# Optimization experiments

Measured on AMD Instinct MI355X. Metric: run time of the kernel, lower is better.

The kernel has to match this reference:

```python
import jax, jax.numpy as jnp
import numpy as np
from jax import lax

C_LIGHT = 3e8
SPATIAL, CROP = 64, 128
BIN_LEN, WALL, SAMP_COEFF, CYCLES = 0.01, 2.0, 2.0, 5
B, D = 2, 1


def _waveconvparam(bin_resolution, virtual_wavelength, cycles):
    samples = int(round(cycles * virtual_wavelength / (C_LIGHT * bin_resolution)))
    num_cycles = samples * (C_LIGHT * bin_resolution) / virtual_wavelength
    sigma = 0.3
    g = np.arange(samples, dtype=np.float64)
    env = np.exp(-(((g - samples / 2.0) / (samples / 2.0)) ** 2) / (2 * sigma ** 2))
    cos_k = np.cos(2 * np.pi * num_cycles * g / samples) * env
    sin_k = np.sin(2 * np.pi * num_cycles * g / samples) * env
    return cos_k, sin_k


def _define_psf(N, M, slope):
    # LCT psf: locus of min |(4 slope)^2 (x^2+y^2) - z|, normalized and circularly shifted
    x = np.arange(2 * N, dtype=np.float64) / (2 * N - 1) * 2 - 1
    z = np.arange(2 * M, dtype=np.float64) / (2 * M - 1) * 2
    gy, gx, gz = np.meshgrid(x, x, z)  # (2N,2N,2M)
    blur = np.abs((4 * slope) ** 2 * (gx ** 2 + gy ** 2) - gz)
    d = (np.abs(blur - blur.min(axis=2, keepdims=True)) < 1e-8).astype(np.float64)
    e = d / np.sqrt(d.sum())
    f = np.roll(np.roll(e, N, axis=0), N, axis=1)
    return np.transpose(f, (2, 0, 1))  # (2M,2N,2N)


def _resampling_operator(M):
    row = M * M
    x = np.arange(1, row + 1, dtype=np.float64)
    mtx = np.zeros((row, M), dtype=np.float64)
    mtx[np.arange(row), np.ceil(np.sqrt(x)).astype(np.int64) - 1] = 1.0
    mtx = mtx / np.sqrt(x)[:, None]
    mtxi = mtx.T.copy()
    for _ in range(int(np.log2(M))):
        mtx = 0.5 * (mtx[0::2] + mtx[1::2])
        mtxi = 0.5 * (mtxi[:, 0::2] + mtxi[:, 1::2])
    return mtx.astype(np.float32), mtxi.astype(np.float32)


def setup_inputs() -> dict:
    key = jax.random.key(0)
    kf, kw, kb = jax.random.split(key, 3)
    bin_res = BIN_LEN / C_LIGHT
    trange = CROP * C_LIGHT * bin_res
    slope = (WALL / 2.0) / trange
    vlam = SAMP_COEFF * 2.0 * (WALL / (SPATIAL - 1))
    cos_k, sin_k = _waveconvparam(bin_res, vlam, CYCLES)
    wave = np.stack([cos_k, sin_k], 0)[:, ::-1][:, None, :].astype(np.float32)  # (2,1,k)
    psf = _define_psf(SPATIAL, CROP, slope)
    invpsf = np.conj(np.fft.fftn(psf))
    mtx, mtxi = _resampling_operator(CROP)
    return {
        "feature": jax.random.normal(kf, (B, D, CROP, SPATIAL, SPATIAL), jnp.float32),
        "conv_w": jax.random.normal(kw, ()) * 0.1 + 1.0,
        "conv_b": jax.random.normal(kb, ()) * 0.1,
        "wave": jnp.asarray(wave),
        "invpsf_real": jnp.asarray(np.real(invpsf).astype(np.float32))[None],
        "invpsf_imag": jnp.asarray(np.imag(invpsf).astype(np.float32))[None],
        "mtx": jnp.asarray(mtx),
        "mtxi": jnp.asarray(mtxi),
    }


def _attention(k1, k2, w, b):
    # SE-style cross attention; Conv3d(1,1,1) on unbatched (C=1,T,H,W) is w*x+b
    T = k2.shape[1]
    pe = jnp.sin(jnp.arange(T, dtype=k2.dtype))  # PE3D with 1 channel -> sin along T
    k2p = k2 + pe[None, :, None, None]
    scal = jnp.mean(w * k1 + b)  # conv + adaptive_avg_pool3d(1), channel dim = 1
    q = (w * k2p + b).reshape(1, 1, -1)
    attn = jax.nn.sigmoid(jax.nn.softmax(scal * q, axis=2)).reshape(k2p.shape)
    return attn * k2p


def _fre_atten2(kernel, w, b):
    _, T, H, W = kernel.shape
    ct, ch, cw = T // 2, H // 2, W // 2
    st, sh, sw = (T - ct) // 2, (H - ch) // 2, (W - cw) // 2
    sl = (slice(None), slice(ct - st, ct + st), slice(ch - sh, ch + sh), slice(cw - sw, cw + sw))
    high = kernel[sl]
    low = jnp.roll(kernel, (ct, ch, cw), axis=(1, 2, 3))[sl]
    l2l = _attention(low, low, w, b)
    l2h = _attention(l2l, high, w, b)
    temp = kernel.at[sl].set(l2h)
    temp = jnp.roll(temp, (ct, ch, cw), axis=(1, 2, 3)).at[sl].set(l2l)
    return jnp.roll(temp, (ct, ch, cw), axis=(1, 2, 3))


def _forward(feature, conv_w, conv_b, wave, invpsf_real, invpsf_imag, mtx, mtxi):
    b, d, T, H, W = feature.shape
    BD = b * d
    k = wave.shape[2]
    # virtual wave conv along time: (BDHW,1,T) x (2,1,k)
    data = feature.reshape(BD, T, H, W).transpose(0, 2, 3, 1).reshape(-1, 1, T)
    conv = lax.conv_general_dilated(data, wave, (1,), [(k // 2, k // 2)],
                                    dimension_numbers=("NCH", "OIH", "NCH"))
    if k % 2 == 0:
        conv = conv[:, :, 1:]
    data2 = conv.reshape(BD, H, W, 2, T).transpose(3, 0, 4, 1, 2).reshape(2 * BD, T, H, W)
    # temporal resampling then zero-pad to 2T,2H,2W
    tmp = jnp.einsum("tm,bmx->btx", mtx, data2.reshape(2 * BD, T, H * W)).reshape(2 * BD, T, H, W)
    datapad = jnp.zeros((2 * BD, 2 * T, 2 * H, 2 * W), feature.dtype).at[:, :T, :H, :W].set(tmp)
    datafre = jnp.fft.fftn(datapad)  # torch.fft.fftn transforms ALL dims incl. batch
    w1 = _fre_atten2(invpsf_real, conv_w, conv_b)
    w2 = _fre_atten2(invpsf_imag, conv_w, conv_b)
    re_real = datafre.real * w1 - datafre.imag * w2
    re_imag = datafre.real * w2 + datafre.imag * w1
    re = jnp.fft.ifftn(lax.complex(re_real, re_imag))
    vol = re[:, :T, :H, :W]
    cr, ci = vol[:BD].real, vol[:BD].imag
    sr, si = vol[BD:].real, vol[BD:].imag
    sum_real = cr ** 2 - ci ** 2 + sr ** 2 - si ** 2
    sum_imag = 2 * cr * ci + 2 * sr * si
    mag = jax.nn.relu((jnp.sqrt(sum_real ** 2 + sum_imag ** 2) + sum_real) * 0.5)
    sq = jnp.sqrt(mag)
    out = jnp.einsum("tm,bmx->btx", mtxi, sq.reshape(BD, T, H * W))
    return out.reshape(b, d, T, H, W)


def reference(feature, conv_w, conv_b, wave, invpsf_real, invpsf_imag, mtx, mtxi):
    return _forward(feature, conv_w, conv_b, wave, invpsf_real, invpsf_imag, mtx, mtxi)
```

## Files before the change

kernel.cpp:

```cpp
#include <hip/hip_runtime.h>

#define BLKE 524288
#define VOLE 4194304
#define TCROP 2097152
#define PI2 6.283185307179586476925286766559

__device__ __forceinline__ float2 cmulf(float2 a, float2 b){
  return make_float2(a.x*b.x - a.y*b.y, a.x*b.y + a.y*b.x);
}
__device__ __forceinline__ float waveSum(float v){
  #pragma unroll
  for (int o=32;o;o>>=1) v += __shfl_xor(v,o);
  return v;
}
__device__ __forceinline__ float waveMaxf(float v){
  #pragma unroll
  for (int o=32;o;o>>=1) v = fmaxf(v,__shfl_xor(v,o));
  return v;
}
__device__ __forceinline__ float waveMinf(float v){
  #pragma unroll
  for (int o=32;o;o>>=1) v = fminf(v,__shfl_xor(v,o));
  return v;
}

__device__ __forceinline__ void bcastReduce5(const float* __restrict__ pA, int kap,
    float& sum, float& mnl, float& mxl, float& mnh, float& mxh, float* sm ){
  int tid = threadIdx.x;
  const float* q = pA + kap*1280 + tid*5;
  float s = q[0], a = q[1], b = q[2], c = q[3], d = q[4];
  s = waveSum(s); a = waveMinf(a); b = waveMaxf(b); c = waveMinf(c); d = waveMaxf(d);
  if ((tid&63)==0){ int w = tid>>6; sm[w]=s; sm[4+w]=a; sm[8+w]=b; sm[12+w]=c; sm[16+w]=d; }
  __syncthreads();
  sum = sm[0]+sm[1]+sm[2]+sm[3];
  mnl = fminf(fminf(sm[4],sm[5]),fminf(sm[6],sm[7]));
  mxl = fmaxf(fmaxf(sm[8],sm[9]),fmaxf(sm[10],sm[11]));
  mnh = fminf(fminf(sm[12],sm[13]),fminf(sm[14],sm[15]));
  mxh = fmaxf(fmaxf(sm[16],sm[17]),fmaxf(sm[18],sm[19]));
}

__device__ __forceinline__ float bcastSum256(const float* __restrict__ p, float* sm ){
  int tid = threadIdx.x;
  float s = waveSum(p[tid]);
  if ((tid&63)==0) sm[tid>>6] = s;
  __syncthreads();
  return sm[0]+sm[1]+sm[2]+sm[3];
}

__global__ void __launch_bounds__(256) kD1(const float* __restrict__ mtx,
                                           const float* __restrict__ wave,
                                           float* __restrict__ M,
                                           const float* __restrict__ Kr,
                                           const float* __restrict__ Ki,
                                           float* __restrict__ Lw, float* __restrict__ Hw,
                                           float* __restrict__ pA){
  __shared__ float spe[128];
  __shared__ float sm[20];
  int bid = blockIdx.x;
  int tid = threadIdx.x;
  if (bid < 512){
    int kap = bid >> 8, bx = bid & 255;
    const float* K = kap ? Ki : Kr;
    if (tid < 128) spe[tid] = sinf((float)tid);
    __syncthreads();
    float sum=0.f, mnl=3.4e38f, mxl=-3.4e38f, mnh=3.4e38f, mxh=-3.4e38f;
    int base = bx*256 + tid;
    #pragma unroll
    for (int it = 0; it < 8; it++){
      int e = base + it*65536;
      int tau = e >> 12, rem = e & 4095, eta = rem >> 6, om = rem & 63;
      float pe = spe[tau];
      float lo = K[(size_t)((tau+192)&255)*16384 + ((eta+96)&127)*128 + ((om+96)&127)];
      float hi = K[(size_t)(tau+64)*16384 + (eta+32)*128 + (om+32)];
      sum += lo;
      float lp = lo+pe, hp = hi+pe;
      Lw[kap*BLKE + e] = lp;
      Hw[kap*BLKE + e] = hp;
      mnl=fminf(mnl,lp); mxl=fmaxf(mxl,lp);
      mnh=fminf(mnh,hp); mxh=fmaxf(mxh,hp);
    }
    sum = waveSum(sum); mnl=waveMinf(mnl); mxl=waveMaxf(mxl); mnh=waveMinf(mnh); mxh=waveMaxf(mxh);
    if ((tid&63)==0){ int w=tid>>6; sm[w]=sum; sm[4+w]=mnl; sm[8+w]=mxl; sm[12+w]=mnh; sm[16+w]=mxh; }
    __syncthreads();
    if (tid==0){
      float* o = pA + kap*1280 + bx*5;
      o[0] = sm[0]+sm[1]+sm[2]+sm[3];
      o[1] = fminf(fminf(sm[4],sm[5]),fminf(sm[6],sm[7]));
      o[2] = fmaxf(fmaxf(sm[8],sm[9]),fmaxf(sm[10],sm[11]));
      o[3] = fminf(fminf(sm[12],sm[13]),fminf(sm[14],sm[15]));
      o[4] = fmaxf(fmaxf(sm[16],sm[17]),fmaxf(sm[18],sm[19]));
    }
  } else {
    int idx = (bid-512)*256 + tid;
    int o = idx >> 14, r = idx & 16383;
    int t = r >> 7, s = r & 127;
    float acc = 0.f;
    int mlo = s-31; if (mlo < 0) mlo = 0;
    int mhi = s+31; if (mhi > 127) mhi = 127;
    for (int m = mlo; m <= mhi; m++) acc += mtx[t*128+m]*wave[o*63 + (s-m+31)];
    M[idx] = acc;
  }
}

__global__ void __launch_bounds__(256) kD2(const float* __restrict__ feat,
                                           const float* __restrict__ M,
                                           float* __restrict__ tmp,
                                           const float* __restrict__ pA,
                                           const float* __restrict__ Lw,
                                           float* __restrict__ pB,
                                           const float* cw, const float* cb){
  __shared__ __align__(16) char smem[16640];
  __shared__ float sm[20], smo[4];
  int bid = blockIdx.x;
  int tid = threadIdx.x;
  if (bid < 512){
    int kap = bid >> 8, bx = bid & 255;
    float sum,mnl,mxl,mnh,mxh;
    bcastReduce5(pA,kap,sum,mnl,mxl,mnh,mxh,sm);
    float w = cw[0], b = cb[0];
    float s1 = w*(sum*(1.0f/BLKE)) + b;
    float a1 = s1*w, c1 = s1*b;
    float mx = (a1>=0.f) ? a1*mxl+c1 : a1*mnl+c1;
    float acc = 0.f;
    int base = kap*BLKE + bx*256 + tid;
    #pragma unroll
    for (int it = 0; it < 8; it++){
      float lp = Lw[base + it*65536];
      acc += expf(a1*lp + c1 - mx);
    }
    acc = waveSum(acc);
    if ((tid&63)==0) smo[tid>>6] = acc;
    __syncthreads();
    if (tid==0) pB[kap*256 + bx] = smo[0]+smo[1]+smo[2]+smo[3];
  } else {
    int e = bid - 512;
    int b = e >> 8, tt = (e >> 6) & 3, xt = e & 63;
    float (*LF)[64] = (float(*)[64])smem;
    float (*LM)[32][33] = (float(*)[32][33])(smem + 8192);
    int xx = tid & 63, tq = tid >> 6;
    float acc0[8] = {}, acc1[8] = {};
    const float* fb = feat + (size_t)b*BLKE;
    for (int sb = 0; sb < 4; sb++){
      #pragma unroll
      for (int j = 0; j < 8; j++){
        int idx = tid + j*256; int s = idx >> 6, x = idx & 63;
        LF[s][x] = fb[(size_t)(sb*32+s)*4096 + xt*64 + x];
      }
      #pragma unroll
      for (int j = 0; j < 8; j++){
        int idx = tid + j*256; int o = idx >> 10, r = idx & 1023;
        int trow = r >> 5, s = r & 31;
        LM[o][trow][s] = M[o*16384 + (tt*32+trow)*128 + sb*32+s];
      }
      __syncthreads();
      for (int s = 0; s < 32; s++){
        float f = LF[s][xx];
        #pragma unroll
        for (int i = 0; i < 8; i++){
          acc0[i] += LM[0][tq*8+i][s]*f;
          acc1[i] += LM[1][tq*8+i][s]*f;
        }
      }
      __syncthreads();
    }
    #pragma unroll
    for (int i = 0; i < 8; i++){
      int t = tt*32 + tq*8 + i;
      tmp[(size_t)(0*2+b)*BLKE + (size_t)t*4096 + xt*64+xx] = acc0[i];
      tmp[(size_t)(1*2+b)*BLKE + (size_t)t*4096 + xt*64+xx] = acc1[i];
    }
  }
}

__global__ void __launch_bounds__(256) kD3(const float* __restrict__ tmp,
                                           float2* __restrict__ Z2,
                                           const float* __restrict__ pA,
                                           const float* __restrict__ pB,
                                           const float* __restrict__ Lw,
                                           float* __restrict__ pC,
                                           const float* cw, const float* cb){
  __shared__ __align__(16) char smem[8832];
  __shared__ float sm[20], smB[4], smo[4];
  int bid = blockIdx.x;
  int tid = threadIdx.x;
  if (bid < 512){
    int kap = bid >> 8, bx = bid & 255;
    float sum,mnl,mxl,mnh,mxh;
    bcastReduce5(pA,kap,sum,mnl,mxl,mnh,mxh,sm);
    float d1 = bcastSum256(pB + kap*256, smB);
    float w = cw[0], b = cb[0];
    float s1 = w*(sum*(1.0f/BLKE)) + b;
    float a1 = s1*w, c1 = s1*b;
    float mx = (a1>=0.f) ? a1*mxl+c1 : a1*mnl+c1;
    float invd = 1.0f/d1;
    float acc = 0.f;
    int base = kap*BLKE + bx*256 + tid;
    #pragma unroll
    for (int it = 0; it < 8; it++){
      float lp = Lw[base + it*65536];
      float p = expf(a1*lp + c1 - mx)*invd;
      acc += lp/(1.f + expf(-p));
    }
    acc = waveSum(acc);
    if ((tid&63)==0) smo[tid>>6] = acc;
    __syncthreads();
    if (tid==0) pC[kap*256 + bx] = smo[0]+smo[1]+smo[2]+smo[3];
  } else {
    int e = bid - 512;
    int b = e >> 11, bx = e & 2047;
    float2 (*bA)[130] = (float2(*)[130])smem;
    float2 (*bB)[130] = (float2(*)[130])(smem + 4160);
    float2* tw = (float2*)(smem + 8320);
    if (tid < 64){
      double ang = -PI2 * (double)tid / 128.0;
      tw[tid] = make_float2((float)cos(ang), (float)sin(ang));
    }
    int l = tid >> 6, lane = tid & 63;
    int line = bx*4 + l;
    int t = line >> 6, h = line & 63;
    const float* pc = tmp + (size_t)b*BLKE + (size_t)t*4096 + h*64;
    const float* ps = tmp + (size_t)(2+b)*BLKE + (size_t)t*4096 + h*64;
    bA[l][lane] = make_float2(pc[lane], ps[lane]);
    bA[l][lane+64] = make_float2(0.f, 0.f);
    __syncthreads();
    float2 (*src)[130] = bA, (*dst)[130] = bB;
    int m = 1;
    #pragma unroll
    for (int st = 0; st < 7; st++){
      int i = lane;
      int jm = i & ~(m-1);
      float2 a = src[l][i], b2 = src[l][i+64];
      float2 s = make_float2(a.x+b2.x, a.y+b2.y);
      float2 d = make_float2(a.x-b2.x, a.y-b2.y);
      dst[l][i+jm]   = s;
      dst[l][i+jm+m] = cmulf(d, tw[jm]);
      __syncthreads();
      float2 (*tp)[130] = src; src = dst; dst = tp;
      m <<= 1;
    }
    float2* outp = Z2 + (size_t)b*TCROP + (size_t)t*16384 + (size_t)h*128;
    outp[lane]    = src[l][lane];
    outp[lane+64] = src[l][lane+64];
  }
}

__global__ void __launch_bounds__(256) kD4(float2* __restrict__ Z2,
                                           const float* __restrict__ pA,
                                           const float* __restrict__ pC,
                                           const float* __restrict__ Hw,
                                           float* __restrict__ pD,
                                           const float* cw, const float* cb){
  __shared__ __align__(16) char smem[33792];
  __shared__ float sm[20], smC[4], smo[4];
  int bid = blockIdx.x;
  int tid = threadIdx.x;
  if (bid < 512){
    int kap = bid >> 8, bx = bid & 255;
    float sum,mnl,mxl,mnh,mxh;
    bcastReduce5(pA,kap,sum,mnl,mxl,mnh,mxh,sm);
    float sl2 = bcastSum256(pC + kap*256, smC);
    float w = cw[0], b = cb[0];
    float s2 = w*(sl2*(1.0f/BLKE)) + b;
    float a2 = s2*w, c2 = s2*b;
    float mx = (a2>=0.f) ? a2*mxh+c2 : a2*mnh+c2;
    float acc = 0.f;
    int base = kap*BLKE + bx*256 + tid;
    #pragma unroll
    for (int it = 0; it < 8; it++){
      float hp = Hw[base + it*65536];
      acc += expf(a2*hp + c2 - mx);
    }
    acc = waveSum(acc);
    if ((tid&63)==0) smo[tid>>6] = acc;
    __syncthreads();
    if (tid==0) pD[kap*256 + bx] = smo[0]+smo[1]+smo[2]+smo[3];
  } else {
    int e = bid - 512;
    int b = e >> 10, bx = e & 1023;
    float2 (*bA)[130] = (float2(*)[130])smem;
    float2 (*bB)[130] = (float2(*)[130])(smem + 16640);
    float2* tw = (float2*)(smem + 33280);
    if (tid < 64){
      double ang = -PI2 * (double)tid / 128.0;
      tw[tid] = make_float2((float)cos(ang), (float)sin(ang));
    }
    float2* Z = Z2 + (size_t)b*TCROP;
    int t = bx >> 3; int w0 = (bx & 7) << 4;
    size_t base = (size_t)t*16384 + w0;
    #pragma unroll
    for (int q = 0; q < 4; q++){
      int idx = q*256 + tid; int wl = idx & 15, hh = idx >> 4;
      bA[wl][hh] = Z[base + (size_t)hh*128 + wl];
      bA[wl][hh+64] = make_float2(0.f, 0.f);
    }
    __syncthreads();
    float2 (*src)[130] = bA, (*dst)[130] = bB;
    int m = 1;
    #pragma unroll
    for (int st = 0; st < 7; st++){
      #pragma unroll
      for (int q = 0; q < 4; q++){
        int g = q*256 + tid; int li = g >> 6; int i = g & 63;
        int jm = i & ~(m-1);
        float2 a = src[li][i], b2 = src[li][i+64];
        float2 s = make_float2(a.x+b2.x, a.y+b2.y);
        float2 d = make_float2(a.x-b2.x, a.y-b2.y);
        dst[li][i+jm]   = s;
        dst[li][i+jm+m] = cmulf(d, tw[jm]);
      }
      __syncthreads();
      float2 (*tp)[130] = src; src = dst; dst = tp;
      m <<= 1;
    }
    #pragma unroll
    for (int q = 0; q < 8; q++){
      int idx = q*256 + tid; int wl = idx & 15, hh = idx >> 4;
      Z[base + (size_t)hh*128 + wl] = src[wl][hh];
    }
  }
}

__device__ __forceinline__ float attnv(float v, float a, float c, float mx, float invd){
  float p = expf(a*v + c - mx)*invd;
  return v / (1.f + expf(-p));
}
__device__ __forceinline__ float2 wcAt(int t, int h, int w,
                                       const float* __restrict__ Kr, const float* __restrict__ Ki,
                                       const float* spe, const float* P){
  size_t off = (size_t)t*16384 + (size_t)h*128 + w;
  float kr = Kr[off], ki = Ki[off];
  bool center = (t>=64 && t<192) && (h>=32 && h<96) && (w>=32 && w<96);
  int tc = (t+64)&255, hc = (h+32)&127, wc = (w+32)&127;
  bool corner = (tc<128) && (hc<64) && (wc<64);
  float2 o;
  if (center){
    float pe = spe[t-64];
    o.x = attnv(kr+pe, P[4],  P[5],  P[6],  P[7]);
    o.y = attnv(ki+pe, P[12], P[13], P[14], P[15]);
  } else if (corner){
    float pe = spe[tc];
    o.x = attnv(kr+pe, P[0], P[1],  P[2],  P[3]);
    o.y = attnv(ki+pe, P[8], P[9],  P[10], P[11]);
  } else {
    o.x = kr; o.y = ki;
  }
  return o;
}

__global__ void __launch_bounds__(256) kWcF(const float* __restrict__ Kr,
                                            const float* __restrict__ Ki,
                                            const float* __restrict__ pA,
                                            const float* __restrict__ pB,
                                            const float* __restrict__ pC,
                                            const float* __restrict__ pD,
                                            const float* cw, const float* cb,
                                            float2* __restrict__ Wc){
  __shared__ float spe[128];
  __shared__ float P[16];
  __shared__ float sm[20], smB[4], smC[4], smD[4];
  int tid = threadIdx.x;
  if (tid < 128) spe[tid] = sinf((float)tid);
  for (int kap = 0; kap < 2; kap++){
    if (kap) __syncthreads();
    float sum,mnl,mxl,mnh,mxh;
    bcastReduce5(pA,kap,sum,mnl,mxl,mnh,mxh,sm);
    float d1  = bcastSum256(pB + kap*256, smB);
    float sl2 = bcastSum256(pC + kap*256, smC);
    float d2  = bcastSum256(pD + kap*256, smD);
    if (tid==0){
      float w = cw[0], b = cb[0];
      float s1 = w*(sum*(1.0f/BLKE)) + b;
      float a1 = s1*w, c1 = s1*b;
      float mx1 = (a1>=0.f) ? a1*mxl+c1 : a1*mnl+c1;
      float s2 = w*(sl2*(1.0f/BLKE)) + b;
      float a2 = s2*w, c2 = s2*b;
      float mx2 = (a2>=0.f) ? a2*mxh+c2 : a2*mnh+c2;
      float* Q = P + kap*8;
      Q[0]=a1; Q[1]=c1; Q[2]=mx1; Q[3]=1.0f/d1;
      Q[4]=a2; Q[5]=c2; Q[6]=mx2; Q[7]=1.0f/d2;
    }
  }
  __syncthreads();
  #pragma unroll
  for (int q = 0; q < 4; q++){
    int idx = blockIdx.x*1024 + q*256 + tid;
    int t = idx >> 14, r = idx & 16383, h = r >> 7, w = r & 127;
    Wc[idx] = wcAt(t, h, w, Kr, Ki, spe, P);
  }
}

__global__ void __launch_bounds__(256) kTfused(const float2* __restrict__ Z2,
                                               float2* __restrict__ U2,
                                               float2* __restrict__ V2,
                                               const float2* __restrict__ Wc){
  __shared__ float2 buf[16][259];
  __shared__ float2 tw[256];
  int tid = threadIdx.x;
  {
    double ang = -PI2 * (double)tid / 256.0;
    tw[tid] = make_float2((float)cos(ang), (float)sin(ang));
  }
  int b = blockIdx.y;
  int bid = blockIdx.x;
  int h = bid >> 3, w0 = (bid & 7) << 4;
  int wl = tid & 15, pq = tid >> 4;
  const float2* Z = Z2 + (size_t)b*TCROP;
  size_t gbase = (size_t)h*128 + w0 + wl;
  #pragma unroll
  for (int q = 0; q < 8; q++){
    int p = q*16 + pq;
    buf[wl][p] = Z[(size_t)p*16384 + gbase];
    buf[wl][p+128] = make_float2(0.f, 0.f);
  }
  __syncthreads();
  #pragma unroll
  for (int st = 0; st < 4; st++){
    const int Q = 64 >> (2*st);
    const int f = 1 << (2*st);
    #pragma unroll
    for (int it = 0; it < 4; it++){
      int u = pq + 16*it;
      int j = u & (Q-1);
      int seg = u >> (6 - 2*st);
      int base = (seg << (8 - 2*st)) + j;
      float2 a0 = buf[wl][base];
      float2 a1 = buf[wl][base+Q];
      float2 a2 = buf[wl][base+2*Q];
      float2 a3 = buf[wl][base+3*Q];
      float2 t0 = make_float2(a0.x+a2.x, a0.y+a2.y);
      float2 t1 = make_float2(a0.x-a2.x, a0.y-a2.y);
      float2 t2 = make_float2(a1.x+a3.x, a1.y+a3.y);
      float2 t3 = make_float2(a1.x-a3.x, a1.y-a3.y);
      float2 z0 = make_float2(t0.x+t2.x, t0.y+t2.y);
      float2 z2 = make_float2(t0.x-t2.x, t0.y-t2.y);
      float2 z1 = make_float2(t1.x+t3.y, t1.y-t3.x);
      float2 z3 = make_float2(t1.x-t3.y, t1.y+t3.x);
      buf[wl][base]     = z0;
      buf[wl][base+Q]   = cmulf(z1, tw[f*j]);
      buf[wl][base+2*Q] = cmulf(z2, tw[2*f*j]);
      buf[wl][base+3*Q] = cmulf(z3, tw[3*f*j]);
    }
    __syncthreads();
  }
  float2 rg[16];
  #pragma unroll
  for (int q = 0; q < 16; q++) rg[q] = buf[wl][q*16 + pq];
  #pragma unroll
  for (int q = 0; q < 16; q++){
    int p = q*16 + pq;
    int kt = ((p&3)<<6) | (((p>>2)&3)<<4) | (((p>>4)&3)<<2) | ((p>>6)&3);
    float2 wc = Wc[(size_t)kt*16384 + (size_t)h*128 + w0 + wl];
    buf[wl][p] = cmulf(rg[q], wc);
  }
  __syncthreads();
  #pragma unroll
  for (int st = 0; st < 4; st++){
    const int Q = 1 << (2*st);
    const int f = 64 >> (2*st);
    #pragma unroll
    for (int it = 0; it < 4; it++){
      int u = pq + 16*it;
      int j = u & (Q-1);
      int seg = u >> (2*st);
      int base = (seg << (2*st + 2)) + j;
      float2 w1 = tw[f*j], w2 = tw[2*f*j], w3 = tw[3*f*j];
      float2 a0 = buf[wl][base];
      float2 r1 = buf[wl][base+Q];
      float2 r2 = buf[wl][base+2*Q];
      float2 r3 = buf[wl][base+3*Q];
      float2 b1 = make_float2(r1.x*w1.x + r1.y*w1.y, r1.y*w1.x - r1.x*w1.y);
      float2 b2 = make_float2(r2.x*w2.x + r2.y*w2.y, r2.y*w2.x - r2.x*w2.y);
      float2 b3 = make_float2(r3.x*w3.x + r3.y*w3.y, r3.y*w3.x - r3.x*w3.y);
      float2 t0 = make_float2(a0.x+b2.x, a0.y+b2.y);
      float2 t1 = make_float2(a0.x-b2.x, a0.y-b2.y);
      float2 t2 = make_float2(b1.x+b3.x, b1.y+b3.y);
      float2 t3 = make_float2(b1.x-b3.x, b1.y-b3.y);
      buf[wl][base]     = make_float2(t0.x+t2.x, t0.y+t2.y);
      buf[wl][base+Q]   = make_float2(t1.x-t3.y, t1.y+t3.x);
      buf[wl][base+2*Q] = make_float2(t0.x-t2.x, t0.y-t2.y);
      buf[wl][base+3*Q] = make_float2(t1.x+t3.y, t1.y-t3.x);
    }
    __syncthreads();
  }
  float2* Uo = U2 + (size_t)b*TCROP;
  #pragma unroll
  for (int q = 0; q < 8; q++){
    int p = q*16 + pq;
    Uo[(size_t)p*16384 + gbase] = buf[wl][p];
  }
  #pragma unroll
  for (int q = 0; q < 16; q++){
    int p = q*16 + pq;
    int kt = ((p&3)<<6) | (((p>>2)&3)<<4) | (((p>>4)&3)<<2) | ((p>>6)&3);
    int tm = (256-kt)&255, hm = (128-h)&127, wm = (128-(w0+wl))&127;
    float2 wc = Wc[(size_t)tm*16384 + (size_t)hm*128 + wm];
    wc.y = -wc.y;
    buf[wl][p] = cmulf(rg[q], wc);
  }
  __syncthreads();
  #pragma unroll
  for (int st = 0; st < 4; st++){
    const int Q = 1 << (2*st);
    const int f = 64 >> (2*st);
    #pragma unroll
    for (int it = 0; it < 4; it++){
      int u = pq + 16*it;
      int j = u & (Q-1);
      int seg = u >> (2*st);
      int base = (seg << (2*st + 2)) + j;
      float2 w1 = tw[f*j], w2 = tw[2*f*j], w3 = tw[3*f*j];
      float2 a0 = buf[wl][base];
      float2 r1 = buf[wl][base+Q];
      float2 r2 = buf[wl][base+2*Q];
      float2 r3 = buf[wl][base+3*Q];
      float2 b1 = make_float2(r1.x*w1.x + r1.y*w1.y, r1.y*w1.x - r1.x*w1.y);
      float2 b2 = make_float2(r2.x*w2.x + r2.y*w2.y, r2.y*w2.x - r2.x*w2.y);
      float2 b3 = make_float2(r3.x*w3.x + r3.y*w3.y, r3.y*w3.x - r3.x*w3.y);
      float2 t0 = make_float2(a0.x+b2.x, a0.y+b2.y);
      float2 t1 = make_float2(a0.x-b2.x, a0.y-b2.y);
      float2 t2 = make_float2(b1.x+b3.x, b1.y+b3.y);
      float2 t3 = make_float2(b1.x-b3.x, b1.y-b3.y);
      buf[wl][base]     = make_float2(t0.x+t2.x, t0.y+t2.y);
      buf[wl][base+Q]   = make_float2(t1.x-t3.y, t1.y+t3.x);
      buf[wl][base+2*Q] = make_float2(t0.x-t2.x, t0.y-t2.y);
      buf[wl][base+3*Q] = make_float2(t1.x+t3.y, t1.y-t3.x);
    }
    __syncthreads();
  }
  float2* Vo = V2 + (size_t)b*TCROP;
  #pragma unroll
  for (int q = 0; q < 8; q++){
    int p = q*16 + pq;
    Vo[(size_t)p*16384 + gbase] = buf[wl][p];
  }
}

__global__ void __launch_bounds__(256) kHi(float2* __restrict__ U2, float2* __restrict__ V2){
  __shared__ float2 bA[16][130], bB[16][130], tw[64];
  int tid = threadIdx.x;
  if (tid < 64){
    double ang = PI2 * (double)tid / 128.0;
    tw[tid] = make_float2((float)cos(ang), (float)sin(ang));
  }
  float2* Z = (blockIdx.z ? V2 : U2) + (size_t)blockIdx.y*TCROP;
  int bid = blockIdx.x;
  int t = bid >> 3; int w0 = (bid & 7) << 4;
  size_t base = (size_t)t*16384 + w0;
  #pragma unroll
  for (int q = 0; q < 8; q++){
    int idx = q*256 + tid; int wl = idx & 15, hh = idx >> 4;
    bA[wl][hh] = Z[base + (size_t)hh*128 + wl];
  }
  __syncthreads();
  float2 (*src)[130] = bA, (*dst)[130] = bB;
  int m = 1;
  #pragma unroll
  for (int st = 0; st < 7; st++){
    #pragma unroll
    for (int q = 0; q < 4; q++){
      int g = q*256 + tid; int li = g >> 6; int i = g & 63;
      int jm = i & ~(m-1);
      float2 a = src[li][i], b2 = src[li][i+64];
      float2 s = make_float2(a.x+b2.x, a.y+b2.y);
      float2 d = make_float2(a.x-b2.x, a.y-b2.y);
      dst[li][i+jm]   = s;
      dst[li][i+jm+m] = cmulf(d, tw[jm]);
    }
    __syncthreads();
    float2 (*tp)[130] = src; src = dst; dst = tp;
    m <<= 1;
  }
  #pragma unroll
  for (int q = 0; q < 4; q++){
    int idx = q*256 + tid; int wl = idx & 15, hh = idx >> 4;
    Z[base + (size_t)hh*128 + wl] = src[wl][hh];
  }
}

__global__ void __launch_bounds__(256) kI3C(const float2* __restrict__ U2,
                                            const float2* __restrict__ V2,
                                            float* __restrict__ sq){
  __shared__ float2 bA[4][130], bB[4][130], tw[64];
  int tid = threadIdx.x;
  if (tid < 64){
    double ang = PI2 * (double)tid / 128.0;
    tw[tid] = make_float2((float)cos(ang), (float)sin(ang));
  }
  int b = blockIdx.y;
  int l = tid >> 6, lane = tid & 63;
  int line = blockIdx.x*4 + l;
  int t = line >> 6, h = line & 63;
  size_t off = (size_t)b*TCROP + (size_t)t*16384 + (size_t)h*128;
  bA[l][lane]    = U2[off + lane];
  bA[l][lane+64] = U2[off + lane + 64];
  __syncthreads();
  float2 (*src)[130] = bA, (*dst)[130] = bB;
  int m = 1;
  #pragma unroll
  for (int st = 0; st < 7; st++){
    int i = lane;
    int jm = i & ~(m-1);
    float2 a = src[l][i], b2 = src[l][i+64];
    float2 s = make_float2(a.x+b2.x, a.y+b2.y);
    float2 d = make_float2(a.x-b2.x, a.y-b2.y);
    dst[l][i+jm]   = s;
    dst[l][i+jm+m] = cmulf(d, tw[jm]);
    __syncthreads();
    float2 (*tp)[130] = src; src = dst; dst = tp;
    m <<= 1;
  }
  float2 y = src[l][lane];
  dst[l][lane]    = V2[off + lane];
  dst[l][lane+64] = V2[off + lane + 64];
  __syncthreads();
  src = dst; dst = (src == bA) ? bB : bA;
  m = 1;
  #pragma unroll
  for (int st = 0; st < 7; st++){
    int i = lane;
    int jm = i & ~(m-1);
    float2 a = src[l][i], b2 = src[l][i+64];
    float2 s = make_float2(a.x+b2.x, a.y+b2.y);
    float2 d = make_float2(a.x-b2.x, a.y-b2.y);
    dst[l][i+jm]   = s;
    dst[l][i+jm+m] = cmulf(d, tw[jm]);
    __syncthreads();
    float2 (*tp)[130] = src; src = dst; dst = tp;
    m <<= 1;
  }
  float2 v = src[l][lane];
  const float sc = 1.0f/(float)VOLE;
  const float sc2 = sc*sc;
  float2 s = cmulf(y, make_float2(v.x, -v.y));
  s.x *= sc2; s.y *= sc2;
  float mag = 0.5f*(sqrtf(s.x*s.x + s.y*s.y) + s.x);
  mag = fmaxf(mag, 0.f);
  sq[(size_t)b*BLKE + (size_t)t*4096 + h*64 + lane] = sqrtf(mag);
}

__global__ void __launch_bounds__(256) kOut(const float* __restrict__ sq,
                                            const float* __restrict__ mtxi,
                                            float* __restrict__ out){
  __shared__ float LF[32][64];
  __shared__ float LM[32][33];
  int b = blockIdx.z, tt = blockIdx.y, xt = blockIdx.x;
  int tid = threadIdx.x;
  int xx = tid & 63, tq = tid >> 6;
  float acc[8] = {};
  const float* fb = sq + (size_t)b*BLKE;
  for (int sb = 0; sb < 4; sb++){
    #pragma unroll
    for (int j = 0; j < 8; j++){
      int idx = tid + j*256; int s = idx >> 6, x = idx & 63;
      LF[s][x] = fb[(size_t)(sb*32+s)*4096 + xt*64 + x];
    }
    #pragma unroll
    for (int j = 0; j < 4; j++){
      int idx = tid + j*256; int trow = idx >> 5, s = idx & 31;
      LM[trow][s] = mtxi[(tt*32+trow)*128 + sb*32+s];
    }
    __syncthreads();
    for (int s = 0; s < 32; s++){
      float f = LF[s][xx];
      #pragma unroll
      for (int i = 0; i < 8; i++) acc[i] += LM[tq*8+i][s]*f;
    }
    __syncthreads();
  }
  #pragma unroll
  for (int i = 0; i < 8; i++){
    int t = tt*32 + tq*8 + i;
    out[(size_t)b*BLKE + (size_t)t*4096 + xt*64+xx] = acc[i];
  }
}

extern "C" void kernel_launch(void* const* d_in, const int* in_sizes, int n_in,
                              void* d_out, int out_size, void* d_ws, size_t ws_size,
                              hipStream_t stream){
  const float* feature = (const float*)d_in[0];
  const float* convW   = (const float*)d_in[1];
  const float* convB   = (const float*)d_in[2];
  const float* wave    = (const float*)d_in[3];
  const float* Kr      = (const float*)d_in[4];
  const float* Ki      = (const float*)d_in[5];
  const float* mtx     = (const float*)d_in[6];
  const float* mtxi    = (const float*)d_in[7];
  float* out = (float*)d_out;
  float* ws  = (float*)d_ws;

  float*  M    = ws;
  float*  pA   = ws + 32832;
  float*  pB   = ws + 35392;
  float*  pC   = ws + 35904;
  float*  pD   = ws + 36416;
  float*  tmp  = ws + 65536;
  float*  sq   = ws + 65536 + 2097152;
  float2* Z2   = (float2*)(ws + 3211264);
  float2* U2   = (float2*)(ws + 11599872);
  float2* V2   = (float2*)(ws + 19988480);
  float2* Wc   = (float2*)(ws + 28377088);
  float*  Lw   = (float*)U2;
  float*  Hw   = ((float*)U2) + 1048576;

  kD1 <<<640,  256, 0, stream>>>(mtx, wave, M, Kr, Ki, Lw, Hw, pA);
  kD2 <<<1024, 256, 0, stream>>>(feature, M, tmp, pA, Lw, pB, convW, convB);
  kD3 <<<4608, 256, 0, stream>>>(tmp, Z2, pA, pB, Lw, pC, convW, convB);
  kD4 <<<2560, 256, 0, stream>>>(Z2, pA, pC, Hw, pD, convW, convB);
  kWcF<<<4096, 256, 0, stream>>>(Kr, Ki, pA, pB, pC, pD, convW, convB, Wc);
  kTfused<<<dim3(1024,2), 256, 0, stream>>>(Z2, U2, V2, Wc);
  kHi<<<dim3(1024,2,2), 256, 0, stream>>>(U2, V2);
  kI3C<<<dim3(2048,2), 256, 0, stream>>>(U2, V2, sq);
  kOut<<<dim3(64,4,2), 256, 0, stream>>>(sq, mtxi, out);
}
```

Baseline: 273.6 us.

## Compute attention weights only for center/corner regions, read raw PSF elsewhere

The weight-building kernel now visits only the two attention-modified regions (center and wrapped corner, each a quarter of the volume in t and h,w) rather than the full 256x128x128 volume. It writes Wc only at those positions. The fused T-FFT kernel picks per element whether to read Wc or the raw Kr/Ki planes, and prefetches both the direct and mirrored weights into registers early so the loads overlap with FFT work. This removes most of the Wc write traffic and kernel work, at the cost of divergent gathers from three arrays and more register pressure in kTfused.

```diff
diff --git a/kernel.cpp b/kernel.cpp
--- a/kernel.cpp
+++ b/kernel.cpp
@@ -324,30 +324,14 @@
   float p = expf(a*v + c - mx)*invd;
   return v / (1.f + expf(-p));
 }
-__device__ __forceinline__ float2 wcAt(int t, int h, int w,
-                                       const float* __restrict__ Kr, const float* __restrict__ Ki,
-                                       const float* spe, const float* P){
-  size_t off = (size_t)t*16384 + (size_t)h*128 + w;
-  float kr = Kr[off], ki = Ki[off];
+__device__ __forceinline__ bool wcRegion(int t, int h, int w){
   bool center = (t>=64 && t<192) && (h>=32 && h<96) && (w>=32 && w<96);
   int tc = (t+64)&255, hc = (h+32)&127, wc = (w+32)&127;
   bool corner = (tc<128) && (hc<64) && (wc<64);
-  float2 o;
-  if (center){
-    float pe = spe[t-64];
-    o.x = attnv(kr+pe, P[4],  P[5],  P[6],  P[7]);
-    o.y = attnv(ki+pe, P[12], P[13], P[14], P[15]);
-  } else if (corner){
-    float pe = spe[tc];
-    o.x = attnv(kr+pe, P[0], P[1],  P[2],  P[3]);
-    o.y = attnv(ki+pe, P[8], P[9],  P[10], P[11]);
-  } else {
-    o.x = kr; o.y = ki;
-  }
-  return o;
-}
-
-__global__ void __launch_bounds__(256) kWcF(const float* __restrict__ Kr,
+  return center || corner;
+}
+
+__global__ void __launch_bounds__(256) kWcR(const float* __restrict__ Kr,
                                             const float* __restrict__ Ki,
                                             const float* __restrict__ pA,
                                             const float* __restrict__ pB,
@@ -381,18 +365,36 @@
     }
   }
   __syncthreads();
-  #pragma unroll
-  for (int q = 0; q < 4; q++){
-    int idx = blockIdx.x*1024 + q*256 + tid;
-    int t = idx >> 14, r = idx & 16383, h = r >> 7, w = r & 127;
-    Wc[idx] = wcAt(t, h, w, Kr, Ki, spe, P);
+  int bid = blockIdx.x;
+  bool corner = (bid >= 512);
+  #pragma unroll
+  for (int k = 0; k < 4; k++){
+    int e = (bid & 511)*1024 + k*256 + tid;
+    int tl = e >> 12, rem = e & 4095, hl = rem >> 6, wl_ = rem & 63;
+    int t, h, w;
+    if (!corner){ t = tl+64; h = hl+32; w = wl_+32; }
+    else        { t = (tl+192)&255; h = (hl+96)&127; w = (wl_+96)&127; }
+    float pe = spe[tl];
+    size_t o = (size_t)t*16384 + (size_t)h*128 + w;
+    float kr = Kr[o], ki = Ki[o];
+    float2 v;
+    if (!corner){
+      v.x = attnv(kr+pe, P[4],  P[5],  P[6],  P[7]);
+      v.y = attnv(ki+pe, P[12], P[13], P[14], P[15]);
+    } else {
+      v.x = attnv(kr+pe, P[0], P[1],  P[2],  P[3]);
+      v.y = attnv(ki+pe, P[8], P[9],  P[10], P[11]);
+    }
+    Wc[o] = v;
   }
 }
 
 __global__ void __launch_bounds__(256) kTfused(const float2* __restrict__ Z2,
                                                float2* __restrict__ U2,
                                                float2* __restrict__ V2,
-                                               const float2* __restrict__ Wc){
+                                               const float2* __restrict__ Wc,
+                                               const float* __restrict__ Kr,
+                                               const float* __restrict__ Ki){
   __shared__ float2 buf[16][259];
   __shared__ float2 tw[256];
   int tid = threadIdx.x;
@@ -404,8 +406,18 @@
   int bid = blockIdx.x;
   int h = bid >> 3, w0 = (bid & 7) << 4;
   int wl = tid & 15, pq = tid >> 4;
+  int wg = w0 + wl;
   const float2* Z = Z2 + (size_t)b*TCROP;
-  size_t gbase = (size_t)h*128 + w0 + wl;
+  size_t gbase = (size_t)h*128 + wg;
+  float2 wcu[16];
+  #pragma unroll
+  for (int q = 0; q < 16; q++){
+    int p = q*16 + pq;
+    int kt = ((p&3)<<6) | (((p>>2)&3)<<4) | (((p>>4)&3)<<2) | ((p>>6)&3);
+    size_t o = (size_t)kt*16384 + (size_t)h*128 + wg;
+    if (wcRegion(kt, h, wg)) wcu[q] = Wc[o];
+    else                     wcu[q] = make_float2(Kr[o], Ki[o]);
+  }
   #pragma unroll
   for (int q = 0; q < 8; q++){
     int p = q*16 + pq;
@@ -448,9 +460,17 @@
   #pragma unroll
   for (int q = 0; q < 16; q++){
     int p = q*16 + pq;
+    buf[wl][p] = cmulf(rg[q], wcu[q]);
+  }
+  float2 wcv[16];
+  #pragma unroll
+  for (int q = 0; q < 16; q++){
+    int p = q*16 + pq;
     int kt = ((p&3)<<6) | (((p>>2)&3)<<4) | (((p>>4)&3)<<2) | ((p>>6)&3);
-    float2 wc = Wc[(size_t)kt*16384 + (size_t)h*128 + w0 + wl];
-    buf[wl][p] = cmulf(rg[q], wc);
+    int tm = (256-kt)&255, hm = (128-h)&127, wm = (128-wg)&127;
+    size_t o = (size_t)tm*16384 + (size_t)hm*128 + wm;
+    if (wcRegion(tm, hm, wm)) wcv[q] = Wc[o];
+    else                      wcv[q] = make_float2(Kr[o], Ki[o]);
   }
   __syncthreads();
   #pragma unroll
@@ -491,9 +511,7 @@
   #pragma unroll
   for (int q = 0; q < 16; q++){
     int p = q*16 + pq;
-    int kt = ((p&3)<<6) | (((p>>2)&3)<<4) | (((p>>4)&3)<<2) | ((p>>6)&3);
-    int tm = (256-kt)&255, hm = (128-h)&127, wm = (128-(w0+wl))&127;
-    float2 wc = Wc[(size_t)tm*16384 + (size_t)hm*128 + wm];
+    float2 wc = wcv[q];
     wc.y = -wc.y;
     buf[wl][p] = cmulf(rg[q], wc);
   }
@@ -706,8 +724,8 @@
   kD2 <<<1024, 256, 0, stream>>>(feature, M, tmp, pA, Lw, pB, convW, convB);
   kD3 <<<4608, 256, 0, stream>>>(tmp, Z2, pA, pB, Lw, pC, convW, convB);
   kD4 <<<2560, 256, 0, stream>>>(Z2, pA, pC, Hw, pD, convW, convB);
-  kWcF<<<4096, 256, 0, stream>>>(Kr, Ki, pA, pB, pC, pD, convW, convB, Wc);
-  kTfused<<<dim3(1024,2), 256, 0, stream>>>(Z2, U2, V2, Wc);
+  kWcR<<<1024, 256, 0, stream>>>(Kr, Ki, pA, pB, pC, pD, convW, convB, Wc);
+  kTfused<<<dim3(1024,2), 256, 0, stream>>>(Z2, U2, V2, Wc, Kr, Ki);
   kHi<<<dim3(1024,2,2), 256, 0, stream>>>(U2, V2);
   kI3C<<<dim3(2048,2), 256, 0, stream>>>(U2, V2, sq);
   kOut<<<dim3(64,4,2), 256, 0, stream>>>(sq, mtxi, out);
```

Measured after the change: 276.0 us. No clear change (+0.9%).

## Fuse H and W inverse FFT passes into one per-plane shared-memory kernel

Applied to the files above, without the earlier changes.

Replaces the separate H-axis inverse FFT kernel (which wrote back to global memory) and the W-axis FFT-plus-combine kernel with one kernel that loads a whole 128x128 complex plane into shared memory. It runs in-place decimation-in-frequency passes along both axes, computes only the needed even-index outputs of the W pass, and uses bit reversal when storing the cropped magnitude. This removes one full global round trip of U2 and V2 and one launch. In exchange it uses 128 KB of LDS per block with 1024 threads, which allows only 256 blocks at one per CU, so occupancy and latency hiding may drop.

```diff
diff --git a/kernel.cpp b/kernel.cpp
--- a/kernel.cpp
+++ b/kernel.cpp
@@ -535,107 +535,91 @@
   }
 }
 
-__global__ void __launch_bounds__(256) kHi(float2* __restrict__ U2, float2* __restrict__ V2){
-  __shared__ float2 bA[16][130], bB[16][130], tw[64];
+__global__ void __launch_bounds__(1024) kPlane(const float2* __restrict__ U2,
+                                               const float2* __restrict__ V2,
+                                               float* __restrict__ sq){
+  __shared__ float2 buf[128][128];
+  __shared__ float2 tw[64];
   int tid = threadIdx.x;
   if (tid < 64){
     double ang = PI2 * (double)tid / 128.0;
     tw[tid] = make_float2((float)cos(ang), (float)sin(ang));
   }
-  float2* Z = (blockIdx.z ? V2 : U2) + (size_t)blockIdx.y*TCROP;
-  int bid = blockIdx.x;
-  int t = bid >> 3; int w0 = (bid & 7) << 4;
-  size_t base = (size_t)t*16384 + w0;
-  #pragma unroll
-  for (int q = 0; q < 8; q++){
-    int idx = q*256 + tid; int wl = idx & 15, hh = idx >> 4;
-    bA[wl][hh] = Z[base + (size_t)hh*128 + wl];
-  }
-  __syncthreads();
-  float2 (*src)[130] = bA, (*dst)[130] = bB;
-  int m = 1;
-  #pragma unroll
-  for (int st = 0; st < 7; st++){
-    #pragma unroll
-    for (int q = 0; q < 4; q++){
-      int g = q*256 + tid; int li = g >> 6; int i = g & 63;
-      int jm = i & ~(m-1);
-      float2 a = src[li][i], b2 = src[li][i+64];
-      float2 s = make_float2(a.x+b2.x, a.y+b2.y);
-      float2 d = make_float2(a.x-b2.x, a.y-b2.y);
-      dst[li][i+jm]   = s;
-      dst[li][i+jm+m] = cmulf(d, tw[jm]);
-    }
-    __syncthreads();
-    float2 (*tp)[130] = src; src = dst; dst = tp;
-    m <<= 1;
-  }
-  #pragma unroll
-  for (int q = 0; q < 4; q++){
-    int idx = q*256 + tid; int wl = idx & 15, hh = idx >> 4;
-    Z[base + (size_t)hh*128 + wl] = src[wl][hh];
-  }
-}
-
-__global__ void __launch_bounds__(256) kI3C(const float2* __restrict__ U2,
-                                            const float2* __restrict__ V2,
-                                            float* __restrict__ sq){
-  __shared__ float2 bA[4][130], bB[4][130], tw[64];
-  int tid = threadIdx.x;
-  if (tid < 64){
-    double ang = PI2 * (double)tid / 128.0;
-    tw[tid] = make_float2((float)cos(ang), (float)sin(ang));
-  }
-  int b = blockIdx.y;
-  int l = tid >> 6, lane = tid & 63;
-  int line = blockIdx.x*4 + l;
-  int t = line >> 6, h = line & 63;
-  size_t off = (size_t)b*TCROP + (size_t)t*16384 + (size_t)h*128;
-  bA[l][lane]    = U2[off + lane];
-  bA[l][lane+64] = U2[off + lane + 64];
-  __syncthreads();
-  float2 (*src)[130] = bA, (*dst)[130] = bB;
-  int m = 1;
-  #pragma unroll
-  for (int st = 0; st < 7; st++){
-    int i = lane;
-    int jm = i & ~(m-1);
-    float2 a = src[l][i], b2 = src[l][i+64];
-    float2 s = make_float2(a.x+b2.x, a.y+b2.y);
-    float2 d = make_float2(a.x-b2.x, a.y-b2.y);
-    dst[l][i+jm]   = s;
-    dst[l][i+jm+m] = cmulf(d, tw[jm]);
-    __syncthreads();
-    float2 (*tp)[130] = src; src = dst; dst = tp;
-    m <<= 1;
-  }
-  float2 y = src[l][lane];
-  dst[l][lane]    = V2[off + lane];
-  dst[l][lane+64] = V2[off + lane + 64];
-  __syncthreads();
-  src = dst; dst = (src == bA) ? bB : bA;
-  m = 1;
-  #pragma unroll
-  for (int st = 0; st < 7; st++){
-    int i = lane;
-    int jm = i & ~(m-1);
-    float2 a = src[l][i], b2 = src[l][i+64];
-    float2 s = make_float2(a.x+b2.x, a.y+b2.y);
-    float2 d = make_float2(a.x-b2.x, a.y-b2.y);
-    dst[l][i+jm]   = s;
-    dst[l][i+jm+m] = cmulf(d, tw[jm]);
-    __syncthreads();
-    float2 (*tp)[130] = src; src = dst; dst = tp;
-    m <<= 1;
-  }
-  float2 v = src[l][lane];
-  const float sc = 1.0f/(float)VOLE;
-  const float sc2 = sc*sc;
-  float2 s = cmulf(y, make_float2(v.x, -v.y));
-  s.x *= sc2; s.y *= sc2;
-  float mag = 0.5f*(sqrtf(s.x*s.x + s.y*s.y) + s.x);
-  mag = fmaxf(mag, 0.f);
-  sq[(size_t)b*BLKE + (size_t)t*4096 + h*64 + lane] = sqrtf(mag);
+  int t = blockIdx.x, b = blockIdx.y;
+  size_t pbase = (size_t)b*TCROP + (size_t)t*16384;
+  float2 keep[4];
+  #pragma unroll
+  for (int phase = 0; phase < 2; phase++){
+    const float2* S = phase ? V2 : U2;
+    #pragma unroll
+    for (int q = 0; q < 16; q++){
+      int e = q*1024 + tid;
+      int h = e >> 7, w = e & 127;
+      buf[h][w] = S[pbase + (size_t)h*128 + w];
+    }
+    __syncthreads();
+    #pragma unroll
+    for (int st = 0; st < 7; st++){
+      const int half = 64 >> st;
+      #pragma unroll
+      for (int q = 0; q < 8; q++){
+        int e = q*1024 + tid;
+        int w = e & 127, bf = e >> 7;
+        int j = bf & (half-1);
+        int blk = bf >> (6-st);
+        int i0 = (blk << (7-st)) + j;
+        float2 a = buf[i0][w], c = buf[i0+half][w];
+        buf[i0][w] = make_float2(a.x+c.x, a.y+c.y);
+        float2 d = make_float2(a.x-c.x, a.y-c.y);
+        buf[i0+half][w] = cmulf(d, tw[j << st]);
+      }
+      __syncthreads();
+    }
+    #pragma unroll
+    for (int st = 0; st < 7; st++){
+      const int half = 64 >> st;
+      #pragma unroll
+      for (int q = 0; q < 4; q++){
+        int e = q*1024 + tid;
+        int j64 = e & 63, r = e >> 6;
+        int p = r*2;
+        int j = j64 & (half-1);
+        int blk = j64 >> (6-st);
+        int i0 = (blk << (7-st)) + j;
+        float2 a = buf[p][i0], c = buf[p][i0+half];
+        buf[p][i0] = make_float2(a.x+c.x, a.y+c.y);
+        float2 d = make_float2(a.x-c.x, a.y-c.y);
+        buf[p][i0+half] = cmulf(d, tw[j << st]);
+      }
+      __syncthreads();
+    }
+    if (phase == 0){
+      #pragma unroll
+      for (int k = 0; k < 4; k++){
+        int e = k*1024 + tid;
+        int r = e >> 6, c = e & 63;
+        keep[k] = buf[2*r][2*c];
+      }
+      __syncthreads();
+    } else {
+      const float sc = 1.0f/(float)VOLE;
+      const float sc2 = sc*sc;
+      #pragma unroll
+      for (int k = 0; k < 4; k++){
+        int e = k*1024 + tid;
+        int r = e >> 6, c = e & 63;
+        float2 v = buf[2*r][2*c];
+        float2 y = keep[k];
+        float2 s = cmulf(y, make_float2(v.x, -v.y));
+        s.x *= sc2; s.y *= sc2;
+        float mag = 0.5f*(sqrtf(s.x*s.x + s.y*s.y) + s.x);
+        mag = fmaxf(mag, 0.f);
+        int hh = __brev((unsigned)r) >> 26;
+        int ww = __brev((unsigned)c) >> 26;
+        sq[(size_t)b*BLKE + (size_t)t*4096 + hh*64 + ww] = sqrtf(mag);
+      }
+    }
+  }
 }
 
 __global__ void __launch_bounds__(256) kOut(const float* __restrict__ sq,
@@ -708,7 +692,6 @@
   kD4 <<<2560, 256, 0, stream>>>(Z2, pA, pC, Hw, pD, convW, convB);
   kWcF<<<4096, 256, 0, stream>>>(Kr, Ki, pA, pB, pC, pD, convW, convB, Wc);
   kTfused<<<dim3(1024,2), 256, 0, stream>>>(Z2, U2, V2, Wc);
-  kHi<<<dim3(1024,2,2), 256, 0, stream>>>(U2, V2);
-  kI3C<<<dim3(2048,2), 256, 0, stream>>>(U2, V2, sq);
+  kPlane<<<dim3(128,2), 1024, 0, stream>>>(U2, V2, sq);
   kOut<<<dim3(64,4,2), 256, 0, stream>>>(sq, mtxi, out);
 }
```

Measured after the change: 302.8 us. 10.7% more time.
